# Performance work log

Hardware: AMD Instinct MI355X
Metric: run time of the kernel (lower is better)

The kernel has to match this reference:

```python
import jax, jax.numpy as jnp
import numpy as np

N_NODES = 1024
N_FEAT = 12        # must equal LOOKBACK (U1 @ B @ U2.T constraint in original code)
LOOKBACK = 12
N_DATA = 8
KSIZE = 2
DILATIONS = [1, 3, 3, 3]
DELTA_MIN = 0.05
TIME_FEATS = 36    # 15 + 5 + 4 + 12


def setup_inputs() -> dict:
    key = jax.random.key(0)
    ks = jax.random.split(key, 21)
    f32 = jnp.float32

    def rn(k, shape, fan_in):
        return jax.random.normal(k, shape, dtype=f32) / np.sqrt(fan_in)

    return {
        'observation': jax.random.normal(ks[0], (N_NODES, N_DATA, LOOKBACK), dtype=f32),
        'time_features': jax.random.normal(ks[1], (TIME_FEATS,), dtype=f32),
        # main FC stack: (n_nodes*n_data) -> fc1 -> fc2 -> n_nodes*n_feat
        'fc_w1': rn(ks[2], (N_NODES * N_DATA, 2048), N_NODES * N_DATA),
        'fc_b1': jnp.zeros((2048,), f32),
        'fc_w2': rn(ks[3], (2048, 2048), 2048),
        'fc_b2': jnp.zeros((2048,), f32),
        'fc_w3': rn(ks[4], (2048, N_NODES * N_FEAT), 2048),
        'fc_b3': jnp.zeros((N_NODES * N_FEAT,), f32),
        # graph conv weights
        'W_forward': rn(ks[5], (KSIZE, N_FEAT, N_FEAT), N_FEAT),
        'W_backward': rn(ks[6], (KSIZE, N_FEAT, N_FEAT), N_FEAT),
        'b': jnp.zeros((N_FEAT,), f32),
        # GraphConstructor params (one fixed set, reused for every adjacency)
        'layer_initial': rn(ks[7], (LOOKBACK, N_NODES), N_NODES),
        'gs_w1': rn(ks[8], (N_NODES, 256), N_NODES),
        'gs_b1': jnp.zeros((256,), f32),
        'gs_w2': rn(ks[9], (256, N_NODES * N_FEAT), 256),
        'gs_b2': jnp.zeros((N_NODES * N_FEAT,), f32),
        'gt_w1': rn(ks[10], (TIME_FEATS, 256), TIME_FEATS),
        'gt_b1': jnp.zeros((256,), f32),
        'gt_w2': rn(ks[11], (256, N_NODES * N_FEAT), 256),
        'gt_b2': jnp.zeros((N_NODES * N_FEAT,), f32),
        'B': jax.random.normal(ks[12], (N_FEAT, N_FEAT), dtype=f32) / N_FEAT,
    }


def _forward(observation, time_features, fc_w1, fc_b1, fc_w2, fc_b2, fc_w3, fc_b3,
             W_forward, W_backward, b, layer_initial,
             gs_w1, gs_b1, gs_w2, gs_b2, gt_w1, gt_b1, gt_w2, gt_b2, B):
    relu = jax.nn.relu

    # fully_connected: observation (N, D, L) -> X (N, F, L)
    obs = jnp.transpose(observation, (2, 0, 1)).reshape(LOOKBACK, -1)  # (L, N*D)
    h = relu(obs @ fc_w1 + fc_b1)
    h = relu(h @ fc_w2 + fc_b2)
    h = relu(h @ fc_w3 + fc_b3)                                        # (L, N*F)
    X0 = jnp.transpose(h.reshape(LOOKBACK, N_NODES, N_FEAT), (1, 2, 0))  # (N, F, L)

    # node embedding U (N, L, F), computed once (graph params fixed)
    sp = relu(relu(layer_initial @ gs_w1 + gs_b1) @ gs_w2 + gs_b2)     # (L, N*F)
    tp = relu(relu(time_features @ gt_w1 + gt_b1) @ gt_w2 + gt_b2)     # (N*F,)
    U = jnp.transpose((sp + tp).reshape(LOOKBACK, N_NODES, N_FEAT), (1, 0, 2))

    adj_cache = {}

    def norm_adj(a, c):
        # normalized adjacency between feature-slices a and c (static ints)
        if (a, c) in adj_cache:
            return adj_cache[(a, c)]
        U1 = U[:, :, a]                      # (N, L)
        U2 = U[:, :, c]                      # (N, L)
        x = U1 @ B @ U2.T                    # (N, N); valid since L == F
        x = jnp.where(x >= DELTA_MIN, x, 0.0)
        A = jax.nn.softmax(x, axis=1)        # torch F.softmax default dim=1 for 2D
        # degree = diag(rowsum); inv(sqrtm(diag)) = diag(1/sqrt(rowsum))
        d = 1.0 / jnp.sqrt(A.sum(-1))
        out = A * d[:, None] * d[None, :]
        adj_cache[(a, c)] = out
        return out

    def conv(X, t):
        Z = jnp.zeros((N_NODES, N_FEAT), jnp.float32)
        for k in range(KSIZE):
            X_t = X[:, :, t - k]             # (N, F)
            L1 = norm_adj(t - k, t)
            L2 = norm_adj(t + k, t)
            x = L1 @ X_t @ W_forward[k] + L2 @ X_t @ W_backward[k] + b
            Z = Z + jax.nn.relu(x)
        return Z

    def conv_layer(X, d):
        cols = []
        for t in range(1, LOOKBACK - 1):
            if t % d == 0:
                cols.append(conv(X, t))
            else:
                cols.append(jnp.zeros((N_NODES, N_FEAT), jnp.float32))
        return jnp.stack(cols, axis=-1)      # (N, F, L-2)

    Z0 = conv_layer(X0, DILATIONS[0])
    Z1 = conv_layer(Z0, DILATIONS[1])
    Z2 = conv_layer(Z1, DILATIONS[2])
    Z3 = conv_layer(Z2, DILATIONS[3])
    return (Z0[:, :, -1], Z1[:, :, -1], Z2[:, :, -1], Z3[:, :, -1])


def reference(observation, time_features, fc_w1, fc_b1, fc_w2, fc_b2, fc_w3, fc_b3,
              W_forward, W_backward, b, layer_initial,
              gs_w1, gs_b1, gs_w2, gs_b2, gt_w1, gt_b1, gt_w2, gt_b2, B):
    return _forward(observation, time_features, fc_w1, fc_b1, fc_w2, fc_b2, fc_w3, fc_b3,
                    W_forward, W_backward, b, layer_initial,
                    gs_w1, gs_b1, gs_w2, gs_b2, gt_w1, gt_b1, gt_w2, gt_b2, B)
```

## Files before the change

kernel.cpp:

```cpp
#include <hip/hip_runtime.h>


#define OFF_OBS   0
#define OFF_SPP   16384
#define OFF_TPH   65536
#define OFF_P1    65792
#define OFF_P2    131328
#define OFF_P3    164096
#define OFF_UP    213248
#define OFF_TPP   1392896
#define OFF_U     1491200
#define OFF_Y     1528064

__global__ void __launch_bounds__(256) k_hidden(
    const float* __restrict__ li, const float* __restrict__ gs_w1,
    const float* __restrict__ tf, const float* __restrict__ gt_w1,
    const float* __restrict__ gt_b1, const float* __restrict__ obs,
    float* __restrict__ obs_ws, float* __restrict__ sp_part,
    float* __restrict__ tp_h)
{
  int b = blockIdx.x, tid = threadIdx.x;
  if (b < 16) {
    __shared__ float lil[12][128];
    int cb = b & 1, kc = b >> 1;
    for (int i = tid; i < 1536; i += 256) {
      int bb = i >> 7, kk = i & 127;
      lil[bb][kk] = li[bb*1024 + kc*128 + kk];
    }
    __syncthreads();
    int col = cb*128 + (tid & 127);
    int kh = tid >> 7;
    float acc[12];
    #pragma unroll
    for (int t=0;t<12;++t) acc[t]=0.f;
    for (int kk = kh*64; kk < kh*64 + 64; ++kk) {
      float w = gs_w1[(size_t)(kc*128 + kk)*256 + col];
      #pragma unroll
      for (int t=0;t<12;++t) acc[t] = fmaf(lil[t][kk], w, acc[t]);
    }
    int c = kc*2 + kh;
    #pragma unroll
    for (int t=0;t<12;++t) sp_part[(c*12 + t)*256 + col] = acc[t];
  } else if (b == 16) {
    float acc = 0.f;
    for (int k = 0; k < 36; ++k)
      acc = fmaf(tf[k], gt_w1[k*256 + tid], acc);
    float v = acc + gt_b1[tid];
    tp_h[tid] = v > 0.f ? v : 0.f;
  } else {
    int g = b - 17;
    for (int i = tid; i < 2048; i += 256) {
      int e = g*2048 + i;
      int tp = e >> 13, k = e & 8191;
      int n = k >> 3, d = k & 7;
      obs_ws[e] = obs[n*96 + d*12 + 9 + tp];
    }
  }
}

template<int KS, int PIN, int P>
__device__ __forceinline__ void gemm_body(
    const float* __restrict__ xin, const float* __restrict__ bias_in,
    const float* __restrict__ W, float* __restrict__ part,
    int N, int K, int bx, int by, float* lx, float* red)
{
  int tid = threadIdx.x;
  int k0 = by * KS;
  for (int i = tid; i < 2*KS; i += 256) {
    int t = i / KS, kk = i - t*KS;
    float v;
    if (PIN == 0) {
      v = xin[t*K + k0 + kk];
    } else {
      v = 0.f;
      const float* p0 = xin + (size_t)(t*K + k0 + kk)*PIN;
      #pragma unroll
      for (int p = 0; p < PIN; ++p) v += p0[p];
    }
    if (bias_in) { v += bias_in[k0 + kk]; v = v > 0.f ? v : 0.f; }
    lx[i] = v;
  }
  __syncthreads();
  int kg = tid >> 5, cg = tid & 31;
  int colbase = bx*128 + cg*4;
  float a0=0,a1=0,a2=0,a3=0,c0=0,c1=0,c2=0,c3=0;
  const int ksub = KS/8;
  for (int kk = kg*ksub; kk < kg*ksub + ksub; ++kk) {
    float4 w = *(const float4*)(W + (size_t)(k0+kk)*N + colbase);
    float x0 = lx[kk], x1 = lx[KS + kk];
    a0=fmaf(x0,w.x,a0); a1=fmaf(x0,w.y,a1); a2=fmaf(x0,w.z,a2); a3=fmaf(x0,w.w,a3);
    c0=fmaf(x1,w.x,c0); c1=fmaf(x1,w.y,c1); c2=fmaf(x1,w.z,c2); c3=fmaf(x1,w.w,c3);
  }
  float* rp = red + (kg*32 + cg)*8;
  rp[0]=a0; rp[1]=a1; rp[2]=a2; rp[3]=a3; rp[4]=c0; rp[5]=c1; rp[6]=c2; rp[7]=c3;
  __syncthreads();
  int cg2 = tid & 31, q = tid >> 5;
  float s = 0.f;
  #pragma unroll
  for (int g = 0; g < 8; ++g) s += red[(g*32 + cg2)*8 + q];
  int t = q >> 2, c = q & 3;
  part[(size_t)(t*N + bx*128 + cg2*4 + c)*P + by] = s;
}

template<int KS, int PIN, int P>
__global__ void __launch_bounds__(256) k_gemm(
    const float* __restrict__ xin, const float* __restrict__ bias_in,
    const float* __restrict__ W, float* __restrict__ part, int N, int K)
{
  __shared__ float lx[2*KS];
  __shared__ float red[2048];
  gemm_body<KS, PIN, P>(xin, bias_in, W, part, N, K, blockIdx.x, blockIdx.y,
                        lx, red);
}

__global__ void __launch_bounds__(256) k_big(
    const float* __restrict__ part2, const float* __restrict__ fc_b2,
    const float* __restrict__ fc_w3, float* __restrict__ part3,
    const float* __restrict__ sp_part, const float* __restrict__ gs_b1,
    const float* __restrict__ tp_h,
    const float* __restrict__ gs_w2, const float* __restrict__ gt_w2,
    float* __restrict__ U_part, float* __restrict__ tp_part)
{
  __shared__ float smem[4096];
  int g = blockIdx.x, tid = threadIdx.x;
  if (g < 192) {
    gemm_body<1024, 8, 2>(part2, fc_b2, fc_w3, part3, 12288, 2048,
                          g >> 1, g & 1, smem, smem + 2048);
  } else {
    float* spl = smem;
    float* tpl = smem + 96;
    int ug = g - 192;
    int n  = (ug & 3)*256 + tid;
    int uy = ug >> 2;
    int k0 = uy*8;
    if (tid < 96) {
      int kk = tid / 12, t = tid % 12;
      float v = gs_b1[k0 + kk];
      #pragma unroll
      for (int c = 0; c < 16; ++c) v += sp_part[(c*12 + t)*256 + k0 + kk];
      spl[kk*12 + t] = v > 0.f ? v : 0.f;
    }
    if (tid < 8) tpl[tid] = tp_h[k0 + tid];
    __syncthreads();
    float sA[3][12];
    float tA[3] = {0.f, 0.f, 0.f};
    #pragma unroll
    for (int ap=0;ap<3;++ap)
      #pragma unroll
      for (int t=0;t<12;++t) sA[ap][t]=0.f;
    #pragma unroll
    for (int kk = 0; kk < 8; ++kk) {
      float4 ws4 = *(const float4*)(gs_w2 + (size_t)(k0+kk)*12288 + 12*n + 8);
      float4 wt4 = *(const float4*)(gt_w2 + (size_t)(k0+kk)*12288 + 12*n + 8);
      float w0 = ws4.y, w1 = ws4.z, w2 = ws4.w;
      #pragma unroll
      for (int t=0;t<12;++t) {
        float s = spl[kk*12 + t];
        sA[0][t] = fmaf(s, w0, sA[0][t]);
        sA[1][t] = fmaf(s, w1, sA[1][t]);
        sA[2][t] = fmaf(s, w2, sA[2][t]);
      }
      float tv = tpl[kk];
      tA[0] = fmaf(tv, wt4.y, tA[0]);
      tA[1] = fmaf(tv, wt4.z, tA[1]);
      tA[2] = fmaf(tv, wt4.w, tA[2]);
    }
    #pragma unroll
    for (int ap=0;ap<3;++ap) {
      #pragma unroll
      for (int t=0;t<12;++t)
        U_part[(size_t)uy*36864 + ap*12288 + n*12 + t] = sA[ap][t];
      tp_part[uy*3072 + n*3 + ap] = tA[ap];
    }
  }
}

__global__ void __launch_bounds__(256) k_mid(
    const float* __restrict__ U_part, const float* __restrict__ tp_part,
    const float* __restrict__ gs_b2, const float* __restrict__ gt_b2,
    float* __restrict__ U,
    const float* __restrict__ part3, const float* __restrict__ fc_b3,
    const float* __restrict__ Wf, const float* __restrict__ Wb,
    float* __restrict__ Y, float* __restrict__ out_tail)
{
  int b = blockIdx.x, tid = threadIdx.x;
  if (b < 144) {
    int i = b*256 + tid;
    float us = 0.f;
    for (int y = 0; y < 32; ++y) us += U_part[(size_t)y*36864 + i];
    int ap = i / 12288, rem = i - ap*12288, n = rem / 12;
    float ts = 0.f;
    for (int y = 0; y < 32; ++y) ts += tp_part[y*3072 + n*3 + ap];
    int c = n*12 + 9 + ap;
    float sv = us + gs_b2[c]; sv = sv > 0.f ? sv : 0.f;
    float tv = ts + gt_b2[c]; tv = tv > 0.f ? tv : 0.f;
    U[i] = sv + tv;
  } else if (b < 148) {
    __shared__ float Ws0[144], Ws1[144], Ws2[144];
    if (tid < 144) {
      Ws0[tid] = Wf[144 + tid];
      Ws1[tid] = Wf[tid] + Wb[tid];
      Ws2[tid] = Wb[144 + tid];
    }
    __syncthreads();
    int n = (b - 144)*256 + tid;
    float X9[12], X10[12];
    #pragma unroll
    for (int f=0; f<12; ++f) {
      float bb = fc_b3[n*12 + f];
      float v9  = part3[(size_t)(n*12 + f)*2]         + part3[(size_t)(n*12 + f)*2 + 1]         + bb;
      float v10 = part3[(size_t)(12288 + n*12 + f)*2] + part3[(size_t)(12288 + n*12 + f)*2 + 1] + bb;
      X9[f]  = v9  > 0.f ? v9  : 0.f;
      X10[f] = v10 > 0.f ? v10 : 0.f;
    }
    #pragma unroll
    for (int g2=0; g2<12; ++g2) {
      float y0=0.f, y1=0.f, y2=0.f;
      #pragma unroll
      for (int f=0; f<12; ++f) {
        y0 = fmaf(X9[f],  Ws0[f*12+g2], y0);
        y1 = fmaf(X10[f], Ws1[f*12+g2], y1);
        y2 = fmaf(X9[f],  Ws2[f*12+g2], y2);
      }
      Y[n*12 + g2]         = y0;
      Y[12288 + n*12 + g2] = y1;
      Y[24576 + n*12 + g2] = y2;
    }
  } else {
    int i = (b - 148)*256 + tid;
    out_tail[i] = 0.f;
  }
}

#define SS 1032
__global__ void __launch_bounds__(256) k_final(
    const float* __restrict__ U, const float* __restrict__ Y,
    const float* __restrict__ Bm, const float* __restrict__ bvec,
    float* __restrict__ out)
{
  __shared__ float sc[6*SS];
  __shared__ float P[2][3][12];
  __shared__ float invS[6];
  __shared__ float Bl[144];
  __shared__ float bl[12];
  int tid = threadIdx.x;
  int i0 = blockIdx.x*2;
  if (tid < 144) Bl[tid] = Bm[tid];
  if (tid < 12)  bl[tid] = bvec[tid];
  __syncthreads();
  if (tid < 72) {
    int r = tid / 36, ap = (tid / 12) % 3, j = tid % 12;
    float s = 0.f;
    #pragma unroll
    for (int t=0;t<12;++t)
      s = fmaf(U[ap*12288 + (i0+r)*12 + t], Bl[t*12 + j], s);
    P[r][ap][j] = s;
  }
  __syncthreads();
  const float* U10 = U + 12288;
  for (int jj = 0; jj < 4; ++jj) {
    int j = tid + jj*256;
    const float4* ur = (const float4*)(U10 + j*12);
    float4 u0 = ur[0], u1 = ur[1], u2 = ur[2];
    float u[12] = {u0.x,u0.y,u0.z,u0.w,u1.x,u1.y,u1.z,u1.w,u2.x,u2.y,u2.z,u2.w};
    #pragma unroll
    for (int r=0;r<2;++r)
      #pragma unroll
      for (int ap=0;ap<3;++ap) {
        float s = 0.f;
        #pragma unroll
        for (int t=0;t<12;++t) s = fmaf(P[r][ap][t], u[t], s);
        sc[(r*3+ap)*SS + j] = (s >= 0.05f) ? s : 0.f;
      }
  }
  __syncthreads();
  int wv = tid >> 6, ln = tid & 63;
  for (int p = wv; p < 6; p += 4) {
    float m = -1e30f;
    for (int q = 0; q < 16; ++q) m = fmaxf(m, sc[p*SS + ln + q*64]);
    #pragma unroll
    for (int o = 32; o > 0; o >>= 1) m = fmaxf(m, __shfl_xor(m, o));
    float sum = 0.f;
    for (int q = 0; q < 16; ++q) {
      int j = ln + q*64;
      float e = __expf(sc[p*SS + j] - m);
      sc[p*SS + j] = e;
      sum += e;
    }
    #pragma unroll
    for (int o = 32; o > 0; o >>= 1) sum += __shfl_xor(sum, o);
    if (ln == 0) invS[p] = 1.f / sum;
  }
  __syncthreads();
  float acc[2][12];
  for (int r = 0; r < 2; ++r)
    for (int f = 0; f < 12; ++f)
      acc[r][f] = 0.f;
  int q3 = tid >> 6, jg = tid & 63;
  if (tid < 192) {
    for (int q = 0; q < 16; ++q) {
      int j = jg + q*64;
      const float4* yr = (const float4*)(Y + q3*12288 + j*12);
      float4 y0 = yr[0], y1 = yr[1], y2 = yr[2];
      float yv[12] = {y0.x,y0.y,y0.z,y0.w,y1.x,y1.y,y1.z,y1.w,y2.x,y2.y,y2.z,y2.w};
      float e0 = sc[(0*3+q3)*SS + j];
      float e1 = sc[(1*3+q3)*SS + j];
      #pragma unroll
      for (int f=0;f<12;++f) {
        acc[0][f] = fmaf(e0, yv[f], acc[0][f]);
        acc[1][f] = fmaf(e1, yv[f], acc[1][f]);
      }
    }
  }
  __syncthreads();
  float* red = sc;
  if (tid < 192) {
    #pragma unroll
    for (int r=0;r<2;++r)
      #pragma unroll
      for (int f=0;f<12;++f)
        red[((q3*2 + r)*12 + f)*64 + jg] = acc[r][f];
  }
  __syncthreads();
  if (tid < 24) {
    int r = tid / 12, f = tid % 12;
    float s0=0.f, s1=0.f, s2=0.f;
    for (int g = 0; g < 64; ++g) {
      s0 += red[((0*2+r)*12+f)*64 + g];
      s1 += red[((1*2+r)*12+f)*64 + g];
      s2 += red[((2*2+r)*12+f)*64 + g];
    }
    float a1v = invS[r*3+1]*s1;
    float a2v = invS[r*3+0]*s0 + invS[r*3+2]*s2;
    float v1 = a1v + bl[f]; v1 = v1>0.f ? v1 : 0.f;
    float v2 = a2v + bl[f]; v2 = v2>0.f ? v2 : 0.f;
    out[(i0+r)*12 + f] = v1 + v2;
  }
}

extern "C" void kernel_launch(void* const* d_in, const int* in_sizes, int n_in,
                              void* d_out, int out_size, void* d_ws, size_t ws_size,
                              hipStream_t stream)
{
  const float* obs   = (const float*)d_in[0];
  const float* tf    = (const float*)d_in[1];
  const float* fc_w1 = (const float*)d_in[2];
  const float* fc_b1 = (const float*)d_in[3];
  const float* fc_w2 = (const float*)d_in[4];
  const float* fc_b2 = (const float*)d_in[5];
  const float* fc_w3 = (const float*)d_in[6];
  const float* fc_b3 = (const float*)d_in[7];
  const float* Wf    = (const float*)d_in[8];
  const float* Wb    = (const float*)d_in[9];
  const float* bvec  = (const float*)d_in[10];
  const float* li    = (const float*)d_in[11];
  const float* gs_w1 = (const float*)d_in[12];
  const float* gs_b1 = (const float*)d_in[13];
  const float* gs_w2 = (const float*)d_in[14];
  const float* gs_b2 = (const float*)d_in[15];
  const float* gt_w1 = (const float*)d_in[16];
  const float* gt_b1 = (const float*)d_in[17];
  const float* gt_w2 = (const float*)d_in[18];
  const float* gt_b2 = (const float*)d_in[19];
  const float* Bm    = (const float*)d_in[20];
  float* out = (float*)d_out;
  float* ws  = (float*)d_ws;

  float* obs_ws  = ws + OFF_OBS;
  float* sp_part = ws + OFF_SPP;
  float* tp_h    = ws + OFF_TPH;
  float* part1   = ws + OFF_P1;
  float* part2   = ws + OFF_P2;
  float* part3   = ws + OFF_P3;
  float* U_part  = ws + OFF_UP;
  float* tp_part = ws + OFF_TPP;
  float* U       = ws + OFF_U;
  float* Y       = ws + OFF_Y;

  k_hidden<<<dim3(25), dim3(256), 0, stream>>>(li, gs_w1, tf, gt_w1, gt_b1, obs,
                                               obs_ws, sp_part, tp_h);
  k_gemm<512, 0, 16><<<dim3(16,16), dim3(256), 0, stream>>>(
      obs_ws, (const float*)nullptr, fc_w1, part1, 2048, 8192);
  k_gemm<256, 16, 8><<<dim3(16,8), dim3(256), 0, stream>>>(
      part1, fc_b1, fc_w2, part2, 2048, 2048);
  k_big<<<dim3(320), dim3(256), 0, stream>>>(part2, fc_b2, fc_w3, part3,
                                             sp_part, gs_b1, tp_h,
                                             gs_w2, gt_w2, U_part, tp_part);
  k_mid<<<dim3(292), dim3(256), 0, stream>>>(U_part, tp_part, gs_b2, gt_b2, U,
                                             part3, fc_b3, Wf, Wb, Y,
                                             out + 12288);
  k_final<<<dim3(512), dim3(256), 0, stream>>>(U, Y, Bm, bvec, out);
}
```

Measured before the change: 312.1 us.

## Fuse observation gather into fc1 GEMM and deepen split-K across FC layers

Removes the separate observation transpose pass by gathering observation values directly inside the fc1 GEMM load, and merges fc1 with the hidden-layer graph-constructor work into one front kernel, dropping a launch. Split-K factors are increased for fc1 (16 to 32), fc2 (8 to 16) and fc3 (2 to 4) to launch more blocks and fill more CUs while streaming the large weight matrices. In exchange, the partial-sum buffers grow and downstream reductions read more partials, and the gathered loads are strided.

```diff
diff --git a/kernel.cpp b/kernel.cpp
--- a/kernel.cpp
+++ b/kernel.cpp
@@ -1,64 +1,17 @@
 #include <hip/hip_runtime.h>
 
 
-#define OFF_OBS   0
-#define OFF_SPP   16384
-#define OFF_TPH   65536
-#define OFF_P1    65792
-#define OFF_P2    131328
-#define OFF_P3    164096
-#define OFF_UP    213248
-#define OFF_TPP   1392896
-#define OFF_U     1491200
-#define OFF_Y     1528064
-
-__global__ void __launch_bounds__(256) k_hidden(
-    const float* __restrict__ li, const float* __restrict__ gs_w1,
-    const float* __restrict__ tf, const float* __restrict__ gt_w1,
-    const float* __restrict__ gt_b1, const float* __restrict__ obs,
-    float* __restrict__ obs_ws, float* __restrict__ sp_part,
-    float* __restrict__ tp_h)
-{
-  int b = blockIdx.x, tid = threadIdx.x;
-  if (b < 16) {
-    __shared__ float lil[12][128];
-    int cb = b & 1, kc = b >> 1;
-    for (int i = tid; i < 1536; i += 256) {
-      int bb = i >> 7, kk = i & 127;
-      lil[bb][kk] = li[bb*1024 + kc*128 + kk];
-    }
-    __syncthreads();
-    int col = cb*128 + (tid & 127);
-    int kh = tid >> 7;
-    float acc[12];
-    #pragma unroll
-    for (int t=0;t<12;++t) acc[t]=0.f;
-    for (int kk = kh*64; kk < kh*64 + 64; ++kk) {
-      float w = gs_w1[(size_t)(kc*128 + kk)*256 + col];
-      #pragma unroll
-      for (int t=0;t<12;++t) acc[t] = fmaf(lil[t][kk], w, acc[t]);
-    }
-    int c = kc*2 + kh;
-    #pragma unroll
-    for (int t=0;t<12;++t) sp_part[(c*12 + t)*256 + col] = acc[t];
-  } else if (b == 16) {
-    float acc = 0.f;
-    for (int k = 0; k < 36; ++k)
-      acc = fmaf(tf[k], gt_w1[k*256 + tid], acc);
-    float v = acc + gt_b1[tid];
-    tp_h[tid] = v > 0.f ? v : 0.f;
-  } else {
-    int g = b - 17;
-    for (int i = tid; i < 2048; i += 256) {
-      int e = g*2048 + i;
-      int tp = e >> 13, k = e & 8191;
-      int n = k >> 3, d = k & 7;
-      obs_ws[e] = obs[n*96 + d*12 + 9 + tp];
-    }
-  }
-}
-
-template<int KS, int PIN, int P>
+#define OFF_SPP   0
+#define OFF_TPH   49152
+#define OFF_P1    65536
+#define OFF_P2    196608
+#define OFF_P3    262144
+#define OFF_UP    393216
+#define OFF_TPP   1572864
+#define OFF_U     1703936
+#define OFF_Y     1740800
+
+template<int KS, int PIN, int P, int GATHER>
 __device__ __forceinline__ void gemm_body(
     const float* __restrict__ xin, const float* __restrict__ bias_in,
     const float* __restrict__ W, float* __restrict__ part,
@@ -69,7 +22,10 @@
   for (int i = tid; i < 2*KS; i += 256) {
     int t = i / KS, kk = i - t*KS;
     float v;
-    if (PIN == 0) {
+    if (GATHER) {
+      int k = k0 + kk;
+      v = xin[(k >> 3)*96 + (k & 7)*12 + 9 + t];
+    } else if (PIN == 0) {
       v = xin[t*K + k0 + kk];
     } else {
       v = 0.f;
@@ -109,8 +65,52 @@
 {
   __shared__ float lx[2*KS];
   __shared__ float red[2048];
-  gemm_body<KS, PIN, P>(xin, bias_in, W, part, N, K, blockIdx.x, blockIdx.y,
-                        lx, red);
+  gemm_body<KS, PIN, P, 0>(xin, bias_in, W, part, N, K,
+                           blockIdx.x, blockIdx.y, lx, red);
+}
+
+__global__ void __launch_bounds__(256) k_front(
+    const float* __restrict__ obs, const float* __restrict__ fc_w1,
+    float* __restrict__ part1,
+    const float* __restrict__ li, const float* __restrict__ gs_w1,
+    const float* __restrict__ tf, const float* __restrict__ gt_w1,
+    const float* __restrict__ gt_b1,
+    float* __restrict__ sp_part, float* __restrict__ tp_h)
+{
+  __shared__ float smem[2560];
+  int b = blockIdx.x, tid = threadIdx.x;
+  if (b < 512) {
+    gemm_body<256, 0, 32, 1>(obs, (const float*)nullptr, fc_w1, part1,
+                             2048, 8192, b & 15, b >> 4, smem, smem + 512);
+  } else if (b < 528) {
+    float (*lil)[128] = (float(*)[128])smem;
+    int sb = b - 512;
+    int cb = sb & 1, kc = sb >> 1;
+    for (int i = tid; i < 1536; i += 256) {
+      int bb = i >> 7, kk = i & 127;
+      lil[bb][kk] = li[bb*1024 + kc*128 + kk];
+    }
+    __syncthreads();
+    int col = cb*128 + (tid & 127);
+    int kh = tid >> 7;
+    float acc[12];
+    #pragma unroll
+    for (int t=0;t<12;++t) acc[t]=0.f;
+    for (int kk = kh*64; kk < kh*64 + 64; ++kk) {
+      float w = gs_w1[(size_t)(kc*128 + kk)*256 + col];
+      #pragma unroll
+      for (int t=0;t<12;++t) acc[t] = fmaf(lil[t][kk], w, acc[t]);
+    }
+    int c = kc*2 + kh;
+    #pragma unroll
+    for (int t=0;t<12;++t) sp_part[(c*12 + t)*256 + col] = acc[t];
+  } else {
+    float acc = 0.f;
+    for (int k = 0; k < 36; ++k)
+      acc = fmaf(tf[k], gt_w1[k*256 + tid], acc);
+    float v = acc + gt_b1[tid];
+    tp_h[tid] = v > 0.f ? v : 0.f;
+  }
 }
 
 __global__ void __launch_bounds__(256) k_big(
@@ -121,15 +121,15 @@
     const float* __restrict__ gs_w2, const float* __restrict__ gt_w2,
     float* __restrict__ U_part, float* __restrict__ tp_part)
 {
-  __shared__ float smem[4096];
+  __shared__ float smem[3072];
   int g = blockIdx.x, tid = threadIdx.x;
-  if (g < 192) {
-    gemm_body<1024, 8, 2>(part2, fc_b2, fc_w3, part3, 12288, 2048,
-                          g >> 1, g & 1, smem, smem + 2048);
+  if (g < 384) {
+    gemm_body<512, 16, 4, 0>(part2, fc_b2, fc_w3, part3, 12288, 2048,
+                             g >> 2, g & 3, smem, smem + 1024);
   } else {
     float* spl = smem;
     float* tpl = smem + 96;
-    int ug = g - 192;
+    int ug = g - 384;
     int n  = (ug & 3)*256 + tid;
     int uy = ug >> 2;
     int k0 = uy*8;
@@ -208,8 +208,11 @@
     #pragma unroll
     for (int f=0; f<12; ++f) {
       float bb = fc_b3[n*12 + f];
-      float v9  = part3[(size_t)(n*12 + f)*2]         + part3[(size_t)(n*12 + f)*2 + 1]         + bb;
-      float v10 = part3[(size_t)(12288 + n*12 + f)*2] + part3[(size_t)(12288 + n*12 + f)*2 + 1] + bb;
+      const float* p9  = part3 + (size_t)(n*12 + f)*4;
+      const float* p10 = part3 + (size_t)(12288 + n*12 + f)*4;
+      float v9 = bb, v10 = bb;
+      #pragma unroll
+      for (int p = 0; p < 4; ++p) { v9 += p9[p]; v10 += p10[p]; }
       X9[f]  = v9  > 0.f ? v9  : 0.f;
       X10[f] = v10 > 0.f ? v10 : 0.f;
     }
@@ -366,7 +369,6 @@
   float* out = (float*)d_out;
   float* ws  = (float*)d_ws;
 
-  float* obs_ws  = ws + OFF_OBS;
   float* sp_part = ws + OFF_SPP;
   float* tp_h    = ws + OFF_TPH;
   float* part1   = ws + OFF_P1;
@@ -377,13 +379,12 @@
   float* U       = ws + OFF_U;
   float* Y       = ws + OFF_Y;
 
-  k_hidden<<<dim3(25), dim3(256), 0, stream>>>(li, gs_w1, tf, gt_w1, gt_b1, obs,
-                                               obs_ws, sp_part, tp_h);
-  k_gemm<512, 0, 16><<<dim3(16,16), dim3(256), 0, stream>>>(
-      obs_ws, (const float*)nullptr, fc_w1, part1, 2048, 8192);
-  k_gemm<256, 16, 8><<<dim3(16,8), dim3(256), 0, stream>>>(
+  k_front<<<dim3(529), dim3(256), 0, stream>>>(obs, fc_w1, part1,
+                                               li, gs_w1, tf, gt_w1, gt_b1,
+                                               sp_part, tp_h);
+  k_gemm<128, 32, 16><<<dim3(16,16), dim3(256), 0, stream>>>(
       part1, fc_b1, fc_w2, part2, 2048, 2048);
-  k_big<<<dim3(320), dim3(256), 0, stream>>>(part2, fc_b2, fc_w3, part3,
+  k_big<<<dim3(512), dim3(256), 0, stream>>>(part2, fc_b2, fc_w3, part3,
                                              sp_part, gs_b1, tp_h,
                                              gs_w2, gt_w2, U_part, tp_part);
   k_mid<<<dim3(292), dim3(256), 0, stream>>>(U_part, tp_part, gs_b2, gt_b2, U,
```

Measured after the change: 294.7 us. 5.6% less time.
